# Kernel tuning notes

Measured on AMD Instinct MI355X. Metric: run time of the kernel, lower is better.

Reference implementation:

```python
import jax, jax.numpy as jnp
import numpy as np

def setup_inputs() -> dict:
    key = jax.random.key(0)
    k1, k2, k3 = jax.random.split(key, 3)
    B, L, H, E = 2, 2048, 16, 64
    queries = jax.random.normal(k1, (B, L, H, E), dtype=jnp.float32)
    keys = jax.random.normal(k2, (B, L, H, E), dtype=jnp.float32)
    values = jax.random.normal(k3, (B, L, H, E), dtype=jnp.float32)
    return {"queries": queries, "keys": keys, "values": values}

def reference(queries, keys, values):
    B, L, H, E = queries.shape
    S = keys.shape[1]
    scale = 1.0 / jnp.sqrt(jnp.asarray(E, dtype=queries.dtype))
    # scores: [B, H, L, S]
    scores = jnp.einsum('blhe,bshe->bhls', queries, keys)
    # causal mask: position l attends to s <= l (TriangularCausalMask triu diag=1 is masked)
    causal = jnp.tril(jnp.ones((L, S), dtype=bool))  # True = keep
    scores = jnp.where(causal[None, None, :, :], scores, -jnp.inf)
    A = jax.nn.softmax(scale * scores, axis=-1)
    # dropout is identity in eval / p=0
    V = jnp.einsum('bhls,bshd->blhd', A, values)
    return V
```

## Files before the change

### kernel.cpp

```cpp
#include <hip/hip_runtime.h>
#include <hip/hip_bf16.h>

typedef __attribute__((ext_vector_type(8))) short short8;
typedef __attribute__((ext_vector_type(4))) float f32x4;
typedef __attribute__((ext_vector_type(2))) unsigned uint2v;

#define MFMA16(a, b, c) __builtin_amdgcn_mfma_f32_16x16x32_bf16((a), (b), (c), 0, 0, 0)

constexpr int Bc = 2, Lc = 2048, Hc = 16, Ec = 64;
constexpr float LOG2E = 1.4426950408889634f;
constexpr float SCALE2 = 0.125f * LOG2E;
constexpr float NEGBIG = -3.0e38f;

union SW { short8 s8; unsigned u[4]; float4 f4; };

__device__ __forceinline__ unsigned cvtpk(float lo, float hi) {
  unsigned r;
  asm("v_cvt_pk_bf16_f32 %0, %1, %2" : "=v"(r) : "v"(lo), "v"(hi));
  return r;
}
__device__ __forceinline__ float exp2v(float x) {
  float r;
  asm("v_exp_f32 %0, %1" : "=v"(r) : "v"(x));
  return r;
}
__device__ __forceinline__ void plswap32(unsigned& a, unsigned& b) {
  uint2v r = __builtin_amdgcn_permlane32_swap(a, b, false, false);
  a = r[0]; b = r[1];
}
__device__ __forceinline__ void plswap16(unsigned& a, unsigned& b) {
  uint2v r = __builtin_amdgcn_permlane16_swap(a, b, false, false);
  a = r[0]; b = r[1];
}
__device__ __forceinline__ float bflymax(float x) {
  unsigned a = __builtin_bit_cast(unsigned, x), b = a;
  plswap16(a, b);
  float y = fmaxf(__builtin_bit_cast(float, a), __builtin_bit_cast(float, b));
  a = __builtin_bit_cast(unsigned, y); b = a;
  plswap32(a, b);
  return fmaxf(__builtin_bit_cast(float, a), __builtin_bit_cast(float, b));
}

__global__ __launch_bounds__(256)
void prep(const float* __restrict__ K, const float* __restrict__ V,
          uint4* __restrict__ Kb, unsigned short* __restrict__ Vt) {
  const int bid = blockIdx.x;
  const int t = threadIdx.x;
  if (bid < 2048) {
    const int i = bid * 256 + t;
    const float4* s = reinterpret_cast<const float4*>(K) + (size_t)i * 2;
    float4 a = s[0], b = s[1];
    uint4 o;
    o.x = cvtpk(a.x, a.y); o.y = cvtpk(a.z, a.w);
    o.z = cvtpk(b.x, b.y); o.w = cvtpk(b.z, b.w);
    Kb[i] = o;
  } else {
    const int vw = (bid - 2048) * 4 + (t >> 6);
    const int l = t & 63;
    const int bh = vw >> 7;
    const int s0 = (vw & 127) * 16;
    const float* vp = V + ((size_t)(bh >> 4) * Lc + s0) * (Hc * Ec) +
                      (bh & 15) * Ec + l;
    float va[16];
    #pragma unroll
    for (int j = 0; j < 16; ++j) va[j] = vp[j * (Hc * Ec)];
    uint4 o0, o1;
    o0.x = cvtpk(va[0], va[1]);   o0.y = cvtpk(va[2], va[3]);
    o0.z = cvtpk(va[4], va[5]);   o0.w = cvtpk(va[6], va[7]);
    o1.x = cvtpk(va[8], va[9]);   o1.y = cvtpk(va[10], va[11]);
    o1.z = cvtpk(va[12], va[13]); o1.w = cvtpk(va[14], va[15]);
    uint4* dst = reinterpret_cast<uint4*>(Vt + ((size_t)vw * 64 + l) * 16);
    dst[0] = o0;
    dst[1] = o1;
  }
}

__global__ __launch_bounds__(512, 2)
void attn_fwd(const float* __restrict__ Qg, const unsigned short* __restrict__ Kb,
              const unsigned short* __restrict__ Vt, float* __restrict__ Og) {
  __shared__ __align__(16) short smem[32768];

  const int bid = blockIdx.x;
  const int pair = bid & 15;
  const int bh = bid >> 4;
  const int h = bh & (Hc - 1);
  const int b = bh >> 4;
  const int iLo = pair;
  const int QbL = iLo * 64;
  const int QbH = (31 - pair) * 64;
  const int RL = (iLo + 2) >> 1;

  const int t = threadIdx.x;
  const int w = t >> 6;
  const int qsub = w & 3;
  const int par = w >> 2;
  const int l = t & 63;
  const int n = l & 15;
  const int g = l >> 4;
  const int sp4 = ((g & 1) << 3) | ((g >> 1) << 2);

  const f32x4 zero4 = {0.f, 0.f, 0.f, 0.f};
  short8 onesv;
  #pragma unroll
  for (int j = 0; j < 8; ++j) onesv[j] = (short)0x3F80;

  short8 qf[2];
  auto loadq = [&](int Qb) {
    const int q = Qb + qsub * 16 + n;
    const float* qp = Qg + ((size_t)(b * Lc + q) * Hc + h) * Ec + g * 8;
    SW a0, a1, b0, b1, r0, r1;
    a0.f4 = reinterpret_cast<const float4*>(qp)[0];
    a1.f4 = reinterpret_cast<const float4*>(qp)[1];
    b0.f4 = reinterpret_cast<const float4*>(qp + 32)[0];
    b1.f4 = reinterpret_cast<const float4*>(qp + 32)[1];
    r0.u[0] = cvtpk(a0.f4.x * SCALE2, a0.f4.y * SCALE2);
    r0.u[1] = cvtpk(a0.f4.z * SCALE2, a0.f4.w * SCALE2);
    r0.u[2] = cvtpk(a1.f4.x * SCALE2, a1.f4.y * SCALE2);
    r0.u[3] = cvtpk(a1.f4.z * SCALE2, a1.f4.w * SCALE2);
    r1.u[0] = cvtpk(b0.f4.x * SCALE2, b0.f4.y * SCALE2);
    r1.u[1] = cvtpk(b0.f4.z * SCALE2, b0.f4.w * SCALE2);
    r1.u[2] = cvtpk(b1.f4.x * SCALE2, b1.f4.y * SCALE2);
    r1.u[3] = cvtpk(b1.f4.z * SCALE2, b1.f4.w * SCALE2);
    qf[0] = r0.s8;
    qf[1] = r1.s8;
  };

  f32x4 acc[4] = {zero4, zero4, zero4, zero4};
  float mrun = NEGBIG, lrun = 0.f;

  const int srow = t >> 2;
  const int prow = (srow & ~12) | ((srow & 4) << 1) | ((srow & 8) >> 1);
  const int kc0 = (t & 3) * 16;
  const int ve = l, vs0 = w * 16;

  float4 kA, kB, vA, vB;

  auto issue = [&](int r0) {
    unsigned koff = (unsigned)((((b * Lc + r0 + srow) * Hc + h) * Ec + kc0) * 2);
    unsigned voff = (unsigned)(((bh * 128 + ((r0 + vs0) >> 4)) * 64 + ve) * 32);
    asm volatile(
      "global_load_dwordx4 %[k0], %[ko], %[kb]\n\t"
      "global_load_dwordx4 %[k1], %[ko], %[kb] offset:16\n\t"
      "global_load_dwordx4 %[v0], %[vo], %[vb]\n\t"
      "global_load_dwordx4 %[v1], %[vo], %[vb] offset:16"
      : [k0]"=v"(kA), [k1]"=v"(kB), [v0]"=v"(vA), [v1]"=v"(vB)
      : [ko]"v"(koff), [vo]"v"(voff), [kb]"s"(Kb), [vb]"s"(Vt)
      : "memory");
  };
  auto commit = [&](int buf) {
    asm volatile("s_waitcnt vmcnt(2)" ::: "memory");
    __builtin_amdgcn_sched_barrier(0);
    short* kt = smem + buf * 8192;
    *reinterpret_cast<short8*>(&kt[(prow * 64 + kc0) ^ ((prow & 7) << 3)]) =
        *reinterpret_cast<short8*>(&kA);
    *reinterpret_cast<short8*>(&kt[(prow * 64 + kc0 + 8) ^ ((prow & 7) << 3)]) =
        *reinterpret_cast<short8*>(&kB);
    asm volatile("s_waitcnt vmcnt(0)" ::: "memory");
    __builtin_amdgcn_sched_barrier(0);
    short* vt = smem + 16384 + buf * 8192;
    const int ch0 = vs0 >> 3;
    *reinterpret_cast<short8*>(&vt[ve * 128 + (((ch0 + 0) ^ (ve & 7)) << 3)]) =
        *reinterpret_cast<short8*>(&vA);
    *reinterpret_cast<short8*>(&vt[ve * 128 + (((ch0 + 1) ^ (ve & 7)) << 3)]) =
        *reinterpret_cast<short8*>(&vB);
  };

  auto round = [&](int Qb, int str, int curb) {
    const int sb = str * 128 + par * 64;
    const int qtop = Qb + qsub * 16;
    if (sb > qtop + 15) return;
    const short* ktb = smem + curb * 8192;
    const short* vtb = smem + 16384 + curb * 8192;

    f32x4 sc[4] = {zero4, zero4, zero4, zero4};
    #pragma unroll
    for (int kc = 0; kc < 2; ++kc) {
      #pragma unroll
      for (int cb = 0; cb < 4; ++cb) {
        const int row = par * 64 + cb * 16 + n;
        const int idx = (row * 64 + kc * 32 + g * 8) ^ ((n & 7) << 3);
        short8 kf = *reinterpret_cast<const short8*>(&ktb[idx]);
        sc[cb] = MFMA16(kf, qf[kc], sc[cb]);
      }
    }

    const int qg = qtop + n;
    if (sb + 63 > qtop) {
      #pragma unroll
      for (int cb = 0; cb < 4; ++cb)
        #pragma unroll
        for (int r = 0; r < 4; ++r)
          if (sb + cb * 16 + sp4 + r > qg) sc[cb][r] = NEGBIG;
    }

    float m8 = fmaxf(fmaxf(fmaxf(sc[0][0], sc[0][1]), fmaxf(sc[0][2], sc[0][3])),
                     fmaxf(fmaxf(sc[1][0], sc[1][1]), fmaxf(sc[1][2], sc[1][3])));
    m8 = fmaxf(m8, fmaxf(fmaxf(fmaxf(sc[2][0], sc[2][1]), fmaxf(sc[2][2], sc[2][3])),
                         fmaxf(fmaxf(sc[3][0], sc[3][1]), fmaxf(sc[3][2], sc[3][3]))));
    m8 = bflymax(m8);

    const bool resc = !__all(m8 <= mrun);
    if (resc) {
      const float mn = fmaxf(mrun, m8);
      const float afac = exp2v(mrun - mn);
      mrun = mn;
      lrun *= afac;
      #pragma unroll
      for (int e4 = 0; e4 < 4; ++e4)
        #pragma unroll
        for (int r = 0; r < 4; ++r) acc[e4][r] *= afac;
    }

    unsigned ua[4], ub[4];
    #pragma unroll
    for (int cb = 0; cb < 4; ++cb) {
      ua[cb] = cvtpk(exp2v(sc[cb][0] - mrun), exp2v(sc[cb][1] - mrun));
      ub[cb] = cvtpk(exp2v(sc[cb][2] - mrun), exp2v(sc[cb][3] - mrun));
    }

    plswap32(ua[0], ua[1]);
    plswap32(ub[0], ub[1]);
    plswap32(ua[2], ua[3]);
    plswap32(ub[2], ub[3]);
    SW pw0, pw1;
    pw0.u[0] = ua[0]; pw0.u[1] = ub[0]; pw0.u[2] = ua[1]; pw0.u[3] = ub[1];
    pw1.u[0] = ua[2]; pw1.u[1] = ub[2]; pw1.u[2] = ua[3]; pw1.u[3] = ub[3];

    #pragma unroll
    for (int e4 = 0; e4 < 4; ++e4) {
      const int e = e4 * 16 + n;
      const int slot0 = (par * 8 + g) ^ (e & 7);
      const int slot1 = (par * 8 + 4 + g) ^ (e & 7);
      short8 vf0 = *reinterpret_cast<const short8*>(&vtb[e * 128 + (slot0 << 3)]);
      acc[e4] = MFMA16(vf0, pw0.s8, acc[e4]);
      short8 vf1 = *reinterpret_cast<const short8*>(&vtb[e * 128 + (slot1 << 3)]);
      acc[e4] = MFMA16(vf1, pw1.s8, acc[e4]);
    }

    f32x4 rs = MFMA16(onesv, pw0.s8, zero4);
    rs = MFMA16(onesv, pw1.s8, rs);
    lrun += rs[0];
  };

  auto merge_store = [&](int Qb, int curb) {
    float* sA = reinterpret_cast<float*>(smem) + curb * 4096;
    float* sB = reinterpret_cast<float*>(smem) + 8192 + curb * 4096;
    __syncthreads();
    const int row = qsub * 16 + n;
    if (par == 1) {
      float* base = (row < 32) ? (sA + row * 68) : (sB + (row - 32) * 68);
      #pragma unroll
      for (int e4 = 0; e4 < 4; ++e4)
        #pragma unroll
        for (int r = 0; r < 4; ++r) base[e4 * 16 + g * 4 + r] = acc[e4][r];
      if (g == 0) {
        sB[2176 + row] = mrun;
        sB[2240 + row] = lrun;
      }
    }
    __syncthreads();
    if (par == 0) {
      const float* base = (row < 32) ? (sA + row * 68) : (sB + (row - 32) * 68);
      const float m1 = sB[2176 + row];
      const float l1 = sB[2240 + row];
      const float mm = fmaxf(mrun, m1);
      const float a0 = exp2v(mrun - mm);
      const float a1 = exp2v(m1 - mm);
      const float inv = 1.0f / (lrun * a0 + l1 * a1);
      const int q = Qb + row;
      float* op = Og + ((size_t)(b * Lc + q) * Hc + h) * Ec;
      #pragma unroll
      for (int e4 = 0; e4 < 4; ++e4) {
        float4 v;
        v.x = (acc[e4][0] * a0 + base[e4 * 16 + g * 4 + 0] * a1) * inv;
        v.y = (acc[e4][1] * a0 + base[e4 * 16 + g * 4 + 1] * a1) * inv;
        v.z = (acc[e4][2] * a0 + base[e4 * 16 + g * 4 + 2] * a1) * inv;
        v.w = (acc[e4][3] * a0 + base[e4 * 16 + g * 4 + 3] * a1) * inv;
        *reinterpret_cast<float4*>(op + e4 * 16 + g * 4) = v;
      }
    }
  };

  constexpr int NRO = 17;
  loadq(QbL);
  issue(0);
  commit(0);
  __syncthreads();

  int cur = 0;
  for (int rd = 0; rd < NRO; ++rd) {
    const bool pre = (rd + 1 < NRO);
    if (pre) {
      const int nrd = rd + 1;
      const int nstr = (nrd < RL) ? nrd : nrd - RL;
      issue(nstr * 128);
    }
    const bool lo = (rd < RL);
    round(lo ? QbL : QbH, lo ? rd : rd - RL, cur);
    if (rd == RL - 1) {
      merge_store(QbL, cur);
      #pragma unroll
      for (int e4 = 0; e4 < 4; ++e4) acc[e4] = zero4;
      mrun = NEGBIG;
      lrun = 0.f;
      loadq(QbH);
    }
    if (pre) commit(cur ^ 1);
    __syncthreads();
    cur ^= 1;
  }

  merge_store(QbH, cur ^ 1);
}

extern "C" void kernel_launch(void* const* d_in, const int* in_sizes, int n_in,
                              void* d_out, int out_size, void* d_ws, size_t ws_size,
                              hipStream_t stream) {
  const float* Q = (const float*)d_in[0];
  const float* K = (const float*)d_in[1];
  const float* V = (const float*)d_in[2];
  float* O = (float*)d_out;
  unsigned short* Kb = (unsigned short*)d_ws;
  unsigned short* Vt = (unsigned short*)((char*)d_ws + (size_t)Bc * Lc * Hc * Ec * 2);
  prep<<<dim3(3072), dim3(256), 0, stream>>>(K, V, (uint4*)Kb, Vt);
  dim3 grid(Bc * Hc * 16);
  attn_fwd<<<grid, dim3(512), 0, stream>>>(Q, Kb, Vt, O);
}
```

Before: 61.30 us.

## Repartition warps: 2 query groups × 4 key splits with 32-row sub-tiles

Changes the warp decomposition from 4 query sub-tiles × 2 key halves to 2 query groups (32 queries each, two 16-row MFMA tiles per warp) × 4 key splits of 32 keys. Each K and V fragment loaded from LDS is now reused for two query tiles, and the upper query tile is skipped when fully masked. The final merge becomes a tree reduction across four key splits through LDS with extra barriers and doubled accumulator registers. The aim is to cut LDS reads per MFMA and to skip causal work more finely, at the cost of more registers and a longer merge phase.

```diff
diff --git a/kernel.cpp b/kernel.cpp
--- a/kernel.cpp
+++ b/kernel.cpp
@@ -79,6 +79,7 @@
 void attn_fwd(const float* __restrict__ Qg, const unsigned short* __restrict__ Kb,
               const unsigned short* __restrict__ Vt, float* __restrict__ Og) {
   __shared__ __align__(16) short smem[32768];
+  __shared__ float mls[2][64], lls[2][64];
 
   const int bid = blockIdx.x;
   const int pair = bid & 15;
@@ -92,8 +93,8 @@
 
   const int t = threadIdx.x;
   const int w = t >> 6;
-  const int qsub = w & 3;
-  const int par = w >> 2;
+  const int qsubg = w & 1;
+  const int spar = w >> 1;
   const int l = t & 63;
   const int n = l & 15;
   const int g = l >> 4;
@@ -104,29 +105,32 @@
   #pragma unroll
   for (int j = 0; j < 8; ++j) onesv[j] = (short)0x3F80;
 
-  short8 qf[2];
+  short8 qf[2][2];
   auto loadq = [&](int Qb) {
-    const int q = Qb + qsub * 16 + n;
-    const float* qp = Qg + ((size_t)(b * Lc + q) * Hc + h) * Ec + g * 8;
-    SW a0, a1, b0, b1, r0, r1;
-    a0.f4 = reinterpret_cast<const float4*>(qp)[0];
-    a1.f4 = reinterpret_cast<const float4*>(qp)[1];
-    b0.f4 = reinterpret_cast<const float4*>(qp + 32)[0];
-    b1.f4 = reinterpret_cast<const float4*>(qp + 32)[1];
-    r0.u[0] = cvtpk(a0.f4.x * SCALE2, a0.f4.y * SCALE2);
-    r0.u[1] = cvtpk(a0.f4.z * SCALE2, a0.f4.w * SCALE2);
-    r0.u[2] = cvtpk(a1.f4.x * SCALE2, a1.f4.y * SCALE2);
-    r0.u[3] = cvtpk(a1.f4.z * SCALE2, a1.f4.w * SCALE2);
-    r1.u[0] = cvtpk(b0.f4.x * SCALE2, b0.f4.y * SCALE2);
-    r1.u[1] = cvtpk(b0.f4.z * SCALE2, b0.f4.w * SCALE2);
-    r1.u[2] = cvtpk(b1.f4.x * SCALE2, b1.f4.y * SCALE2);
-    r1.u[3] = cvtpk(b1.f4.z * SCALE2, b1.f4.w * SCALE2);
-    qf[0] = r0.s8;
-    qf[1] = r1.s8;
-  };
-
-  f32x4 acc[4] = {zero4, zero4, zero4, zero4};
-  float mrun = NEGBIG, lrun = 0.f;
+    #pragma unroll
+    for (int qi = 0; qi < 2; ++qi) {
+      const int q = Qb + qsubg * 32 + qi * 16 + n;
+      const float* qp = Qg + ((size_t)(b * Lc + q) * Hc + h) * Ec + g * 8;
+      SW a0, a1, b0, b1, r0, r1;
+      a0.f4 = reinterpret_cast<const float4*>(qp)[0];
+      a1.f4 = reinterpret_cast<const float4*>(qp)[1];
+      b0.f4 = reinterpret_cast<const float4*>(qp + 32)[0];
+      b1.f4 = reinterpret_cast<const float4*>(qp + 32)[1];
+      r0.u[0] = cvtpk(a0.f4.x * SCALE2, a0.f4.y * SCALE2);
+      r0.u[1] = cvtpk(a0.f4.z * SCALE2, a0.f4.w * SCALE2);
+      r0.u[2] = cvtpk(a1.f4.x * SCALE2, a1.f4.y * SCALE2);
+      r0.u[3] = cvtpk(a1.f4.z * SCALE2, a1.f4.w * SCALE2);
+      r1.u[0] = cvtpk(b0.f4.x * SCALE2, b0.f4.y * SCALE2);
+      r1.u[1] = cvtpk(b0.f4.z * SCALE2, b0.f4.w * SCALE2);
+      r1.u[2] = cvtpk(b1.f4.x * SCALE2, b1.f4.y * SCALE2);
+      r1.u[3] = cvtpk(b1.f4.z * SCALE2, b1.f4.w * SCALE2);
+      qf[qi][0] = r0.s8;
+      qf[qi][1] = r1.s8;
+    }
+  };
+
+  f32x4 acc[2][4] = {{zero4, zero4, zero4, zero4}, {zero4, zero4, zero4, zero4}};
+  float mrun[2] = {NEGBIG, NEGBIG}, lrun[2] = {0.f, 0.f};
 
   const int srow = t >> 2;
   const int prow = (srow & ~12) | ((srow & 4) << 1) | ((srow & 8) >> 1);
@@ -165,118 +169,143 @@
         *reinterpret_cast<short8*>(&vB);
   };
 
+  auto smx = [&](f32x4 (&S)[2], f32x4 (&A)[4], float& M, float& L,
+                 int qtop, int sb) -> SW {
+    if (sb + 31 > qtop) {
+      #pragma unroll
+      for (int cb = 0; cb < 2; ++cb)
+        #pragma unroll
+        for (int r = 0; r < 4; ++r)
+          if (sb + cb * 16 + sp4 + r > qtop + n) S[cb][r] = NEGBIG;
+    }
+    float m8 = fmaxf(fmaxf(fmaxf(S[0][0], S[0][1]), fmaxf(S[0][2], S[0][3])),
+                     fmaxf(fmaxf(S[1][0], S[1][1]), fmaxf(S[1][2], S[1][3])));
+    m8 = bflymax(m8);
+    const bool resc = !__all(m8 <= M);
+    if (resc) {
+      const float mn = fmaxf(M, m8);
+      const float af = exp2v(M - mn);
+      M = mn;
+      L *= af;
+      #pragma unroll
+      for (int e4 = 0; e4 < 4; ++e4)
+        #pragma unroll
+        for (int r = 0; r < 4; ++r) A[e4][r] *= af;
+    }
+    unsigned ua0 = cvtpk(exp2v(S[0][0] - M), exp2v(S[0][1] - M));
+    unsigned ub0 = cvtpk(exp2v(S[0][2] - M), exp2v(S[0][3] - M));
+    unsigned ua1 = cvtpk(exp2v(S[1][0] - M), exp2v(S[1][1] - M));
+    unsigned ub1 = cvtpk(exp2v(S[1][2] - M), exp2v(S[1][3] - M));
+    plswap32(ua0, ua1);
+    plswap32(ub0, ub1);
+    SW pw;
+    pw.u[0] = ua0; pw.u[1] = ub0; pw.u[2] = ua1; pw.u[3] = ub1;
+    f32x4 rs = MFMA16(onesv, pw.s8, zero4);
+    L += rs[0];
+    return pw;
+  };
+
   auto round = [&](int Qb, int str, int curb) {
-    const int sb = str * 128 + par * 64;
-    const int qtop = Qb + qsub * 16;
-    if (sb > qtop + 15) return;
+    const int sb = str * 128 + spar * 32;
+    const int qtopg = Qb + qsubg * 32;
+    if (sb > qtopg + 31) return;
+    const bool act0 = (sb <= qtopg + 15);
     const short* ktb = smem + curb * 8192;
     const short* vtb = smem + 16384 + curb * 8192;
 
-    f32x4 sc[4] = {zero4, zero4, zero4, zero4};
+    f32x4 sc[2][2] = {{zero4, zero4}, {zero4, zero4}};
     #pragma unroll
     for (int kc = 0; kc < 2; ++kc) {
       #pragma unroll
-      for (int cb = 0; cb < 4; ++cb) {
-        const int row = par * 64 + cb * 16 + n;
+      for (int cb = 0; cb < 2; ++cb) {
+        const int row = spar * 32 + cb * 16 + n;
         const int idx = (row * 64 + kc * 32 + g * 8) ^ ((n & 7) << 3);
         short8 kf = *reinterpret_cast<const short8*>(&ktb[idx]);
-        sc[cb] = MFMA16(kf, qf[kc], sc[cb]);
-      }
-    }
-
-    const int qg = qtop + n;
-    if (sb + 63 > qtop) {
-      #pragma unroll
-      for (int cb = 0; cb < 4; ++cb)
-        #pragma unroll
-        for (int r = 0; r < 4; ++r)
-          if (sb + cb * 16 + sp4 + r > qg) sc[cb][r] = NEGBIG;
-    }
-
-    float m8 = fmaxf(fmaxf(fmaxf(sc[0][0], sc[0][1]), fmaxf(sc[0][2], sc[0][3])),
-                     fmaxf(fmaxf(sc[1][0], sc[1][1]), fmaxf(sc[1][2], sc[1][3])));
-    m8 = fmaxf(m8, fmaxf(fmaxf(fmaxf(sc[2][0], sc[2][1]), fmaxf(sc[2][2], sc[2][3])),
-                         fmaxf(fmaxf(sc[3][0], sc[3][1]), fmaxf(sc[3][2], sc[3][3]))));
-    m8 = bflymax(m8);
-
-    const bool resc = !__all(m8 <= mrun);
-    if (resc) {
-      const float mn = fmaxf(mrun, m8);
-      const float afac = exp2v(mrun - mn);
-      mrun = mn;
-      lrun *= afac;
-      #pragma unroll
-      for (int e4 = 0; e4 < 4; ++e4)
-        #pragma unroll
-        for (int r = 0; r < 4; ++r) acc[e4][r] *= afac;
-    }
-
-    unsigned ua[4], ub[4];
-    #pragma unroll
-    for (int cb = 0; cb < 4; ++cb) {
-      ua[cb] = cvtpk(exp2v(sc[cb][0] - mrun), exp2v(sc[cb][1] - mrun));
-      ub[cb] = cvtpk(exp2v(sc[cb][2] - mrun), exp2v(sc[cb][3] - mrun));
-    }
-
-    plswap32(ua[0], ua[1]);
-    plswap32(ub[0], ub[1]);
-    plswap32(ua[2], ua[3]);
-    plswap32(ub[2], ub[3]);
-    SW pw0, pw1;
-    pw0.u[0] = ua[0]; pw0.u[1] = ub[0]; pw0.u[2] = ua[1]; pw0.u[3] = ub[1];
-    pw1.u[0] = ua[2]; pw1.u[1] = ub[2]; pw1.u[2] = ua[3]; pw1.u[3] = ub[3];
+        sc[1][cb] = MFMA16(kf, qf[1][kc], sc[1][cb]);
+        if (act0) sc[0][cb] = MFMA16(kf, qf[0][kc], sc[0][cb]);
+      }
+    }
+
+    SW pw1 = smx(sc[1], acc[1], mrun[1], lrun[1], qtopg + 16, sb);
+    SW pw0{};
+    if (act0) pw0 = smx(sc[0], acc[0], mrun[0], lrun[0], qtopg, sb);
 
     #pragma unroll
     for (int e4 = 0; e4 < 4; ++e4) {
       const int e = e4 * 16 + n;
-      const int slot0 = (par * 8 + g) ^ (e & 7);
-      const int slot1 = (par * 8 + 4 + g) ^ (e & 7);
-      short8 vf0 = *reinterpret_cast<const short8*>(&vtb[e * 128 + (slot0 << 3)]);
-      acc[e4] = MFMA16(vf0, pw0.s8, acc[e4]);
-      short8 vf1 = *reinterpret_cast<const short8*>(&vtb[e * 128 + (slot1 << 3)]);
-      acc[e4] = MFMA16(vf1, pw1.s8, acc[e4]);
-    }
-
-    f32x4 rs = MFMA16(onesv, pw0.s8, zero4);
-    rs = MFMA16(onesv, pw1.s8, rs);
-    lrun += rs[0];
-  };
-
+      const int slot = (spar * 4 + g) ^ (e & 7);
+      short8 vf = *reinterpret_cast<const short8*>(&vtb[e * 128 + (slot << 3)]);
+      acc[1][e4] = MFMA16(vf, pw1.s8, acc[1][e4]);
+      if (act0) acc[0][e4] = MFMA16(vf, pw0.s8, acc[0][e4]);
+    }
+  };
+
+  auto wpart = [&](float* reg, int mreg) {
+    #pragma unroll
+    for (int qi = 0; qi < 2; ++qi) {
+      const int row = qsubg * 32 + qi * 16 + n;
+      #pragma unroll
+      for (int e4 = 0; e4 < 4; ++e4) {
+        const int eo = (e4 * 16 + g * 4) ^ ((n & 7) << 2);
+        float4 v;
+        v.x = acc[qi][e4][0]; v.y = acc[qi][e4][1];
+        v.z = acc[qi][e4][2]; v.w = acc[qi][e4][3];
+        *reinterpret_cast<float4*>(&reg[row * 64 + eo]) = v;
+      }
+      if (g == 0) { mls[mreg][row] = mrun[qi]; lls[mreg][row] = lrun[qi]; }
+    }
+  };
+  auto mpart = [&](const float* reg, int mreg) {
+    #pragma unroll
+    for (int qi = 0; qi < 2; ++qi) {
+      const int row = qsubg * 32 + qi * 16 + n;
+      const float m1 = mls[mreg][row];
+      const float l1 = lls[mreg][row];
+      const float mm = fmaxf(mrun[qi], m1);
+      const float a0 = exp2v(mrun[qi] - mm);
+      const float a1 = exp2v(m1 - mm);
+      mrun[qi] = mm;
+      lrun[qi] = lrun[qi] * a0 + l1 * a1;
+      #pragma unroll
+      for (int e4 = 0; e4 < 4; ++e4) {
+        const int eo = (e4 * 16 + g * 4) ^ ((n & 7) << 2);
+        float4 pv = *reinterpret_cast<const float4*>(&reg[row * 64 + eo]);
+        acc[qi][e4][0] = acc[qi][e4][0] * a0 + pv.x * a1;
+        acc[qi][e4][1] = acc[qi][e4][1] * a0 + pv.y * a1;
+        acc[qi][e4][2] = acc[qi][e4][2] * a0 + pv.z * a1;
+        acc[qi][e4][3] = acc[qi][e4][3] * a0 + pv.w * a1;
+      }
+    }
+  };
   auto merge_store = [&](int Qb, int curb) {
-    float* sA = reinterpret_cast<float*>(smem) + curb * 4096;
-    float* sB = reinterpret_cast<float*>(smem) + 8192 + curb * 4096;
-    __syncthreads();
-    const int row = qsub * 16 + n;
-    if (par == 1) {
-      float* base = (row < 32) ? (sA + row * 68) : (sB + (row - 32) * 68);
-      #pragma unroll
-      for (int e4 = 0; e4 < 4; ++e4)
+    float* regA = reinterpret_cast<float*>(smem + curb * 8192);
+    float* regB = reinterpret_cast<float*>(smem + 16384 + curb * 8192);
+    __syncthreads();
+    if (spar == 1) wpart(regA, 0);
+    if (spar == 3) wpart(regB, 1);
+    __syncthreads();
+    if (spar == 0) mpart(regA, 0);
+    if (spar == 2) mpart(regB, 1);
+    __syncthreads();
+    if (spar == 2) wpart(regA, 0);
+    __syncthreads();
+    if (spar == 0) {
+      mpart(regA, 0);
+      #pragma unroll
+      for (int qi = 0; qi < 2; ++qi) {
+        const float inv = 1.0f / lrun[qi];
+        const int row = qsubg * 32 + qi * 16 + n;
+        const int q = Qb + row;
+        float* op = Og + ((size_t)(b * Lc + q) * Hc + h) * Ec;
         #pragma unroll
-        for (int r = 0; r < 4; ++r) base[e4 * 16 + g * 4 + r] = acc[e4][r];
-      if (g == 0) {
-        sB[2176 + row] = mrun;
-        sB[2240 + row] = lrun;
-      }
-    }
-    __syncthreads();
-    if (par == 0) {
-      const float* base = (row < 32) ? (sA + row * 68) : (sB + (row - 32) * 68);
-      const float m1 = sB[2176 + row];
-      const float l1 = sB[2240 + row];
-      const float mm = fmaxf(mrun, m1);
-      const float a0 = exp2v(mrun - mm);
-      const float a1 = exp2v(m1 - mm);
-      const float inv = 1.0f / (lrun * a0 + l1 * a1);
-      const int q = Qb + row;
-      float* op = Og + ((size_t)(b * Lc + q) * Hc + h) * Ec;
-      #pragma unroll
-      for (int e4 = 0; e4 < 4; ++e4) {
-        float4 v;
-        v.x = (acc[e4][0] * a0 + base[e4 * 16 + g * 4 + 0] * a1) * inv;
-        v.y = (acc[e4][1] * a0 + base[e4 * 16 + g * 4 + 1] * a1) * inv;
-        v.z = (acc[e4][2] * a0 + base[e4 * 16 + g * 4 + 2] * a1) * inv;
-        v.w = (acc[e4][3] * a0 + base[e4 * 16 + g * 4 + 3] * a1) * inv;
-        *reinterpret_cast<float4*>(op + e4 * 16 + g * 4) = v;
+        for (int e4 = 0; e4 < 4; ++e4) {
+          float4 v;
+          v.x = acc[qi][e4][0] * inv;
+          v.y = acc[qi][e4][1] * inv;
+          v.z = acc[qi][e4][2] * inv;
+          v.w = acc[qi][e4][3] * inv;
+          *reinterpret_cast<float4*>(op + e4 * 16 + g * 4) = v;
+        }
       }
     }
   };
@@ -300,9 +329,12 @@
     if (rd == RL - 1) {
       merge_store(QbL, cur);
       #pragma unroll
-      for (int e4 = 0; e4 < 4; ++e4) acc[e4] = zero4;
-      mrun = NEGBIG;
-      lrun = 0.f;
+      for (int qi = 0; qi < 2; ++qi) {
+        #pragma unroll
+        for (int e4 = 0; e4 < 4; ++e4) acc[qi][e4] = zero4;
+        mrun[qi] = NEGBIG;
+        lrun[qi] = 0.f;
+      }
       loadq(QbH);
     }
     if (pre) commit(cur ^ 1);
```

New measurement: 74.05 us. 20.8% more time.
